# Optimization experiments

Hardware: AMD Instinct MI355X
Metric: run time of the kernel (lower is better)

## Reference

```python
import jax, jax.numpy as jnp
import numpy as np
import math

N_SPIXELS = 256
N_ITER = 5
TAU = 0.01
R = 1          # candidate_radius
NORMALIZE = True


def _unfold(x, kh, kw, ph, pw, sh, sw):
    """torch.nn.functional.unfold, returning (b, c, kh, kw, oh, ow)."""
    b, c, H, W = x.shape
    xp = jnp.pad(x, ((0, 0), (0, 0), (ph, ph), (pw, pw)))
    oh = (H + 2 * ph - kh) // sh + 1
    ow = (W + 2 * pw - kw) // sw + 1
    rows = jnp.arange(oh)[:, None] * sh + jnp.arange(kh)[None, :]   # (oh, kh)
    cols = jnp.arange(ow)[:, None] * sw + jnp.arange(kw)[None, :]   # (ow, kw)
    p = xp[:, :, rows][:, :, :, :, cols]    # (b, c, oh, kh, ow, kw)
    return p.transpose(0, 1, 3, 5, 2, 4)    # (b, c, kh, kw, oh, ow)


def _l2norm(t):
    return t / jnp.linalg.norm(t, axis=1, keepdims=True)


def _forward(x):
    b, c, H, W = x.shape
    hs = int(math.sqrt(N_SPIXELS * H / W))
    ws = int(math.sqrt(N_SPIXELS * W / H))
    sh = (H + hs - 1) // hs
    sw = (W + ws - 1) // ws
    # adaptive_avg_pool2d: H, W chosen divisible by hs, ws -> exact block mean
    clst = x.reshape(b, c, hs, H // hs, ws, W // ws).mean(axis=(3, 5))
    if NORMALIZE:
        x = _l2norm(x)
        clst = _l2norm(clst)
    # pad to multiple of (hs, ws): zero for the chosen shapes
    nr = 2 * R + 1
    s2p = None
    for _ in range(N_ITER):
        # update_clst_feats: overlapping unfold over (3*sh, 3*sw) window
        up = _unfold(x, sh * nr, sw * nr, sh * R, sw * R, sh, sw)    # (b,c,3sh,3sw,hs,ws)
        up = up.reshape(b, c, sh * nr * sw * nr, hs, ws)
        sim = jnp.einsum('bcphw,bchw->bphw', up, clst)
        sim = jnp.where(sim == 0, -jnp.inf, sim)                     # mask padded pixels
        s2p = jax.nn.softmax(sim / TAU, axis=1)
        clst = jnp.einsum('bphw,bcphw->bchw', s2p, up)
        if NORMALIZE:
            clst = _l2norm(clst)
    # compute_elem_to_center_assignment
    cand = _unfold(clst, nr, nr, R, R, 1, 1).reshape(b, c, nr * nr, hs * ws)
    # non-overlapping unfold of x with kernel == stride: pure reshape
    uef = x.reshape(b, c, hs, sh, ws, sw).transpose(0, 1, 3, 5, 2, 4)
    uef = uef.reshape(b, c, sh * sw, hs * ws)
    sim = jnp.einsum('bkcn,bkpn->bcpn', cand, uef)   # (b, nr^2, sh*sw, hs*ws)
    # non-overlapping fold back to (H, W)
    sim = sim.reshape(b, nr * nr, sh, sw, hs, ws).transpose(0, 1, 4, 2, 5, 3)
    sim = sim.reshape(b, nr * nr, H, W)
    sim = jnp.where(sim == 0, -jnp.inf, sim)         # mask padded candidate clusters
    p2s = jax.nn.softmax(sim / TAU, axis=1)
    return clst, p2s, s2p


def setup_inputs() -> dict:
    key = jax.random.key(0)
    x = jax.random.normal(key, (2, 32, 256, 256), dtype=jnp.float32)
    return {"x": x}


def reference(x):
    return _forward(x)
```

## Files before the change

### kernel.cpp

```cpp
#include <hip/hip_runtime.h>
#include <math.h>

#define TAU_INV 100.0f
#define SHIFTED_EXP(s) expf(((s) - 0.5f) * TAU_INV)

__device__ inline float combine_one(const float* __restrict__ Sin,
                                    const float* __restrict__ dpin,
                                    int b, int ti, int tj, int c) {
    float acc = 0.f, den = 0.f;
    if (ti >= 0 && ti < 16 && tj >= 0 && tj < 16) {
#pragma unroll
        for (int u = 0; u < 9; ++u) {
            int oy = u / 3 - 1, ox = u % 3 - 1;
            int ii = ti + oy, jj = tj + ox;
            if (ii >= 0 && ii < 16 && jj >= 0 && jj < 16) {
                int src = ((b * 256 + ii * 16 + jj) * 9) + (1 - oy) * 3 + (1 - ox);
                acc += Sin[(size_t)src * 32 + c];
                den += dpin[src];
            }
        }
    }
    float mean = (den > 0.f) ? acc / den : 0.f;
    float p = mean * mean;
#pragma unroll
    for (int k = 16; k >= 1; k >>= 1) p += __shfl_xor(p, k);
    return (p > 0.f) ? mean * (1.0f / sqrtf(p)) : 0.f;
}

__global__ __launch_bounds__(256) void prep_init_kernel(const float* __restrict__ x,
                                                        float* __restrict__ xn,
                                                        float* __restrict__ clst0) {
    int blk = blockIdx.x;
    int b = blk >> 8;
    int cell = blk & 255;
    int ci = cell >> 4, cj = cell & 15;
    int t = threadIdx.x;
    int py = t >> 4, px = t & 15;
    int y = ci * 16 + py, xx = cj * 16 + px;
    int rem = y * 256 + xx;

    __shared__ float sraw[256 * 33];
    __shared__ float red[256];

    const float* xb = x + (size_t)b * (32 * 65536);
    float v[32];
    float ss = 0.f;
#pragma unroll
    for (int c = 0; c < 32; ++c) {
        float tv = xb[c * 65536 + rem];
        v[c] = tv;
        ss += tv * tv;
        sraw[t * 33 + c] = tv;
    }
    float rn = 1.0f / sqrtf(ss);
    float4* outp = (float4*)(xn + ((size_t)b * 65536 + rem) * 32);
#pragma unroll
    for (int q = 0; q < 8; ++q)
        outp[q] = make_float4(v[4*q]*rn, v[4*q+1]*rn, v[4*q+2]*rn, v[4*q+3]*rn);

    __syncthreads();
    int c = t & 31, pg = t >> 5;
    float acc = 0.f;
#pragma unroll
    for (int k = 0; k < 32; ++k) acc += sraw[(pg * 32 + k) * 33 + c];
    red[t] = acc;
    __syncthreads();
    if (t < 128) red[t] += red[t + 128];
    __syncthreads();
    if (t < 64) red[t] += red[t + 64];
    __syncthreads();
    if (t < 32) {
        float m = (red[t] + red[t + 32]) * (1.0f / 256.0f);
        float p = m * m;
#pragma unroll
        for (int k = 16; k >= 1; k >>= 1) p += __shfl_xor(p, k);
        clst0[(size_t)blk * 32 + t] = m * (1.0f / sqrtf(p));
    }
}

__global__ __launch_bounds__(256) void accum9c_kernel(const float* __restrict__ xn,
                                                      const float* __restrict__ clst0,
                                                      const float* __restrict__ Sin,
                                                      const float* __restrict__ dpin,
                                                      float* __restrict__ Sout,
                                                      float* __restrict__ dpout,
                                                      float* __restrict__ clstin5,
                                                      int it) {
    int blk = blockIdx.x;
    int b = blk >> 8;
    int cell = blk & 255;
    int bi = cell >> 4, bj = cell & 15;
    int t = threadIdx.x;

    __shared__ float sclst[9][32];
    __shared__ float se[9][256];
    __shared__ float sacc[8][9][32];
    __shared__ float sdw[4][9];

    if (it == 0) {
        for (int u = t; u < 288; u += 256) {
            int q = u >> 5, c = u & 31;
            int ii = bi + q / 3 - 1, jj = bj + q % 3 - 1;
            float v = 0.f;
            if (ii >= 0 && ii < 16 && jj >= 0 && jj < 16)
                v = clst0[((size_t)(b * 256 + ii * 16 + jj)) * 32 + c];
            sclst[q][c] = v;
        }
    } else {
        {
            int q = t >> 5, c = t & 31;
            float v = combine_one(Sin, dpin, b, bi + q / 3 - 1, bj + q % 3 - 1, c);
            sclst[q][c] = v;
            if (it == 4 && q == 4)
                clstin5[(size_t)blk * 32 + c] = v;
        }
        if (t < 32)
            sclst[8][t] = combine_one(Sin, dpin, b, bi + 1, bj + 1, t);
    }
    __syncthreads();

    int y = bi * 16 + (t >> 4), xx = bj * 16 + (t & 15);
    const float4* f4 = (const float4*)(xn + ((size_t)(b * 65536 + y * 256 + xx)) * 32);
    float fv[32];
#pragma unroll
    for (int q = 0; q < 8; ++q) {
        float4 v = f4[q];
        fv[4*q] = v.x; fv[4*q+1] = v.y; fv[4*q+2] = v.z; fv[4*q+3] = v.w;
    }

    int wid = t >> 6, lane = t & 63;
#pragma unroll
    for (int q = 0; q < 9; ++q) {
        float s = 0.f;
#pragma unroll
        for (int c = 0; c < 32; ++c) s += fv[c] * sclst[q][c];
        float ev = (s == 0.f) ? 0.f : SHIFTED_EXP(s);
        se[q][t] = ev;
        float d = ev;
#pragma unroll
        for (int k = 32; k >= 1; k >>= 1) d += __shfl_xor(d, k);
        if (lane == 0) sdw[wid][q] = d;
    }
    __syncthreads();
    if (t < 9) dpout[blk * 9 + t] = sdw[0][t] + sdw[1][t] + sdw[2][t] + sdw[3][t];

    {
        int c = t & 31, pg = t >> 5;
        const float* base = xn + ((size_t)(b * 65536 + bi * 16 * 256 + bj * 16)) * 32;
        float acc[9];
#pragma unroll
        for (int q = 0; q < 9; ++q) acc[q] = 0.f;
#pragma unroll
        for (int k = 0; k < 32; ++k) {
            int p = pg * 32 + k;
            float xv = base[(size_t)(p >> 4) * 8192 + (p & 15) * 32 + c];
#pragma unroll
            for (int q = 0; q < 9; ++q) acc[q] = fmaf(se[q][p], xv, acc[q]);
        }
#pragma unroll
        for (int q = 0; q < 9; ++q) sacc[pg][q][c] = acc[q];
    }
    __syncthreads();

    {
        int q = t >> 5, cc = t & 31;
        float s8 = 0.f;
#pragma unroll
        for (int g = 0; g < 8; ++g) s8 += sacc[g][q][cc];
        Sout[((size_t)blk * 9 + q) * 32 + cc] = s8;
        if (t < 32) {
            float s9 = 0.f;
#pragma unroll
            for (int g = 0; g < 8; ++g) s9 += sacc[g][8][t];
            Sout[((size_t)blk * 9 + 8) * 32 + t] = s9;
        }
    }
}

__global__ __launch_bounds__(256) void tail_kernel(const float* __restrict__ xn,
                                                   const float* __restrict__ Sin,
                                                   const float* __restrict__ dpin,
                                                   const float* __restrict__ clstin5,
                                                   float* __restrict__ out_clst,
                                                   float* __restrict__ out_p2s,
                                                   float* __restrict__ out_s2p) {
    int blk = blockIdx.x;
    int b = blk >> 8;
    int cell = blk & 255;
    int ci = cell >> 4, cj = cell & 15;
    int t = threadIdx.x;

    __shared__ float sx[256 * 33];
    __shared__ float sclst[9][32];
    __shared__ float srd[256];

    {
        int q = t >> 5, c = t & 31;
        float v = combine_one(Sin, dpin, b, ci + q / 3 - 1, cj + q % 3 - 1, c);
        sclst[q][c] = v;
        if (q == 4)
            out_clst[((size_t)b * 32 + c) * 256 + cell] = v;
    }
    if (t < 32)
        sclst[8][t] = combine_one(Sin, dpin, b, ci + 1, cj + 1, t);

    for (int u = t; u < 8192; u += 256)
        sx[(u >> 5) * 33 + (u & 31)] = clstin5[(size_t)b * 8192 + u];

    {
        int i = t >> 4, j = t & 15;
        float den = 0.f;
#pragma unroll
        for (int u = 0; u < 9; ++u) {
            int oy = u / 3 - 1, ox = u % 3 - 1;
            int ii = i + oy, jj = j + ox;
            if (ii >= 0 && ii < 16 && jj >= 0 && jj < 16)
                den += dpin[((b * 256 + ii * 16 + jj) * 9) + (1 - oy) * 3 + (1 - ox)];
        }
        srd[t] = 1.0f / den;
    }
    __syncthreads();

    {
        int i = t >> 4, j = t & 15;
        const float* cl = sx + t * 33;
        float rd = srd[t];
#pragma unroll
        for (int u = 0; u < 9; ++u) {
            int p = cell * 9 + u;
            int ky = p / 48, kx = p % 48;
            int yy = i * 16 - 16 + ky;
            int xq = j * 16 - 16 + kx;
            float val = 0.f;
            if (yy >= 0 && yy < 256 && xq >= 0 && xq < 256) {
                const float* f = xn + ((size_t)(b * 65536 + yy * 256 + xq)) * 32;
                float s = 0.f;
#pragma unroll
                for (int c = 0; c < 32; ++c) s += f[c] * cl[c];
                if (s != 0.f) val = SHIFTED_EXP(s) * rd;
            }
            out_s2p[(size_t)(b * 2304 + p) * 256 + t] = val;
        }
    }

    {
        int py = t >> 4, px = t & 15;
        int rem = (ci * 16 + py) * 256 + cj * 16 + px;
        const float4* f4 = (const float4*)(xn + ((size_t)b * 65536 + rem) * 32);
        float fv[32];
#pragma unroll
        for (int q = 0; q < 8; ++q) {
            float4 v = f4[q];
            fv[4*q] = v.x; fv[4*q+1] = v.y; fv[4*q+2] = v.z; fv[4*q+3] = v.w;
        }
        float l[9];
        float mx = -INFINITY;
#pragma unroll
        for (int q = 0; q < 9; ++q) {
            float s = 0.f;
#pragma unroll
            for (int c = 0; c < 32; ++c) s += fv[c] * sclst[q][c];
            l[q] = (s == 0.f) ? -INFINITY : s * TAU_INV;
            mx = fmaxf(mx, l[q]);
        }
        float e[9], sum = 0.f;
#pragma unroll
        for (int q = 0; q < 9; ++q) {
            e[q] = (l[q] == -INFINITY) ? 0.f : expf(l[q] - mx);
            sum += e[q];
        }
        float rs = 1.0f / sum;
#pragma unroll
        for (int q = 0; q < 9; ++q)
            out_p2s[((size_t)b * 9 + q) * 65536 + rem] = e[q] * rs;
    }
}

extern "C" void kernel_launch(void* const* d_in, const int* in_sizes, int n_in,
                              void* d_out, int out_size, void* d_ws, size_t ws_size,
                              hipStream_t stream) {
    const float* x = (const float*)d_in[0];
    float* out = (float*)d_out;

    float* out_clst = out;
    float* out_p2s  = out + 16384;
    float* out_s2p  = out + 16384 + 1179648;

    float* ws = (float*)d_ws;
    float* xn      = ws;
    float* clst0   = xn + 4194304;
    float* Sa      = clst0 + 16384;
    float* Sb      = Sa + 147456;
    float* dpa     = Sb + 147456;
    float* dpb     = dpa + 4608;
    float* clstin5 = dpb + 4608;

    prep_init_kernel<<<512, 256, 0, stream>>>(x, xn, clst0);

    float* Sin = Sa;  float* dpin = dpa;
    float* Sout = Sb; float* dpout = dpb;
    for (int it = 0; it < 5; ++it) {
        accum9c_kernel<<<512, 256, 0, stream>>>(xn, clst0, Sin, dpin,
                                                Sout, dpout, clstin5, it);
        float* ts = Sin; Sin = Sout; Sout = ts;
        float* td = dpin; dpin = dpout; dpout = td;
    }
    tail_kernel<<<512, 256, 0, stream>>>(xn, Sin, dpin, clstin5,
                                         out_clst, out_p2s, out_s2p);
}
```

Baseline: 114.0 us.

## Stage pixel features in shared memory and remap tail s2p work per offset

```diff
diff --git a/kernel.cpp b/kernel.cpp
--- a/kernel.cpp
+++ b/kernel.cpp
@@ -92,6 +92,7 @@
     int bi = cell >> 4, bj = cell & 15;
     int t = threadIdx.x;
 
+    __shared__ float sx[256 * 33];
     __shared__ float sclst[9][32];
     __shared__ float se[9][256];
     __shared__ float sacc[8][9][32];
@@ -117,7 +118,6 @@
         if (t < 32)
             sclst[8][t] = combine_one(Sin, dpin, b, bi + 1, bj + 1, t);
     }
-    __syncthreads();
 
     int y = bi * 16 + (t >> 4), xx = bj * 16 + (t & 15);
     const float4* f4 = (const float4*)(xn + ((size_t)(b * 65536 + y * 256 + xx)) * 32);
@@ -127,6 +127,9 @@
         float4 v = f4[q];
         fv[4*q] = v.x; fv[4*q+1] = v.y; fv[4*q+2] = v.z; fv[4*q+3] = v.w;
     }
+#pragma unroll
+    for (int c = 0; c < 32; ++c) sx[t * 33 + c] = fv[c];
+    __syncthreads();
 
     int wid = t >> 6, lane = t & 63;
 #pragma unroll
@@ -146,14 +149,13 @@
 
     {
         int c = t & 31, pg = t >> 5;
-        const float* base = xn + ((size_t)(b * 65536 + bi * 16 * 256 + bj * 16)) * 32;
         float acc[9];
 #pragma unroll
         for (int q = 0; q < 9; ++q) acc[q] = 0.f;
 #pragma unroll
         for (int k = 0; k < 32; ++k) {
             int p = pg * 32 + k;
-            float xv = base[(size_t)(p >> 4) * 8192 + (p & 15) * 32 + c];
+            float xv = sx[p * 33 + c];
 #pragma unroll
             for (int q = 0; q < 9; ++q) acc[q] = fmaf(se[q][p], xv, acc[q]);
         }
@@ -187,25 +189,40 @@
     int blk = blockIdx.x;
     int b = blk >> 8;
     int cell = blk & 255;
-    int ci = cell >> 4, cj = cell & 15;
+    int ky0 = cell >> 4, kx0 = cell & 15;
     int t = threadIdx.x;
 
     __shared__ float sx[256 * 33];
+    __shared__ float L[256 * 33];
     __shared__ float sclst[9][32];
     __shared__ float srd[256];
 
     {
         int q = t >> 5, c = t & 31;
-        float v = combine_one(Sin, dpin, b, ci + q / 3 - 1, cj + q % 3 - 1, c);
+        float v = combine_one(Sin, dpin, b, ky0 + q / 3 - 1, kx0 + q % 3 - 1, c);
         sclst[q][c] = v;
         if (q == 4)
             out_clst[((size_t)b * 32 + c) * 256 + cell] = v;
     }
     if (t < 32)
-        sclst[8][t] = combine_one(Sin, dpin, b, ci + 1, cj + 1, t);
+        sclst[8][t] = combine_one(Sin, dpin, b, ky0 + 1, kx0 + 1, t);
 
     for (int u = t; u < 8192; u += 256)
         sx[(u >> 5) * 33 + (u & 31)] = clstin5[(size_t)b * 8192 + u];
+
+    {
+        int r = t >> 4, s = t & 15;
+        const float4* f4 = (const float4*)(xn +
+            ((size_t)(b * 65536 + (16 * r + ky0) * 256 + 16 * s + kx0)) * 32);
+#pragma unroll
+        for (int q = 0; q < 8; ++q) {
+            float4 v = f4[q];
+            L[t * 33 + 4*q]     = v.x;
+            L[t * 33 + 4*q + 1] = v.y;
+            L[t * 33 + 4*q + 2] = v.z;
+            L[t * 33 + 4*q + 3] = v.w;
+        }
+    }
 
     {
         int i = t >> 4, j = t & 15;
@@ -226,26 +243,27 @@
         const float* cl = sx + t * 33;
         float rd = srd[t];
 #pragma unroll
-        for (int u = 0; u < 9; ++u) {
-            int p = cell * 9 + u;
-            int ky = p / 48, kx = p % 48;
-            int yy = i * 16 - 16 + ky;
-            int xq = j * 16 - 16 + kx;
-            float val = 0.f;
-            if (yy >= 0 && yy < 256 && xq >= 0 && xq < 256) {
-                const float* f = xn + ((size_t)(b * 65536 + yy * 256 + xq)) * 32;
-                float s = 0.f;
-#pragma unroll
-                for (int c = 0; c < 32; ++c) s += f[c] * cl[c];
-                if (s != 0.f) val = SHIFTED_EXP(s) * rd;
+        for (int a = 0; a < 3; ++a) {
+#pragma unroll
+            for (int bb = 0; bb < 3; ++bb) {
+                int r = i + a - 1, s2 = j + bb - 1;
+                float val = 0.f;
+                if (r >= 0 && r < 16 && s2 >= 0 && s2 < 16) {
+                    const float* f = L + (r * 16 + s2) * 33;
+                    float s = 0.f;
+#pragma unroll
+                    for (int c = 0; c < 32; ++c) s += f[c] * cl[c];
+                    if (s != 0.f) val = SHIFTED_EXP(s) * rd;
+                }
+                int p = (ky0 + 16 * a) * 48 + kx0 + 16 * bb;
+                out_s2p[(size_t)(b * 2304 + p) * 256 + t] = val;
             }
-            out_s2p[(size_t)(b * 2304 + p) * 256 + t] = val;
         }
     }
 
     {
         int py = t >> 4, px = t & 15;
-        int rem = (ci * 16 + py) * 256 + cj * 16 + px;
+        int rem = (ky0 * 16 + py) * 256 + kx0 * 16 + px;
         const float4* f4 = (const float4*)(xn + ((size_t)b * 65536 + rem) * 32);
         float fv[32];
 #pragma unroll
```

Result: faster. 101.8 us (-10.6%).
